# Kernel tuning notes

Hardware: AMD Instinct MI355X
Metric: run time of the kernel (lower is better)

The kernel has to match this reference:

```python
import jax, jax.numpy as jnp
import numpy as np

N_NODES = 100000
N_EDGES = 1600000
D_FEAT = 64


def setup_inputs() -> dict:
    key = jax.random.key(0)
    k1, k2, k3 = jax.random.split(key, 3)
    h = jax.random.normal(k1, (N_NODES, D_FEAT), dtype=jnp.float32)
    src = jax.random.randint(k2, (N_EDGES,), 0, N_NODES, dtype=jnp.int32)
    dst = jax.random.randint(k3, (N_EDGES,), 0, N_NODES, dtype=jnp.int32)
    edge_index = jnp.stack([src, dst], axis=0)  # [2, E]
    return {"h": h, "edge_index": edge_index}


def reference(h, edge_index):
    # EdgePassing: message = src node features (gather along edges)
    # Max_aggregation: per-dst-node max over incoming messages (segment max)
    src, dst = edge_index[0], edge_index[1]
    msgs = h[src]  # [E, D] gathered mailbox, never densified per-node
    agg = jax.ops.segment_max(msgs, dst, num_segments=N_NODES)  # [N, D]
    # DGL leaves nodes with no incoming messages at zero; segment_max yields -inf
    return jnp.where(jnp.isneginf(agg), jnp.zeros_like(agg), agg)
```

## Files before the change

kernel.cpp:

```cpp
#include <hip/hip_runtime.h>
#include <stdint.h>

#define D_FEAT 64
#define NEG_INF_BITS 0xFF800000u
#define ENC_NEG_INF  0x007FFFFFu
#define NPB 64
#define BSHIFT 6
#define BM_BLOCK 256
#define MAXB 2048
#define PL_BLOCKS 64
#define PL_THREADS 1024

__device__ __forceinline__ unsigned enc_f32(float v) {
    unsigned b = __float_as_uint(v);
    return ((int)b >= 0) ? (b ^ 0x80000000u) : ~b;
}
__device__ __forceinline__ unsigned dec_bits(unsigned u) {
    if (u == ENC_NEG_INF) return 0u;
    return (u & 0x80000000u) ? (u ^ 0x80000000u) : ~u;
}

__global__ void hist_kernel(const int* __restrict__ dst, int* __restrict__ hist,
                            int E, int B, int aligned4) {
    __shared__ int lh[MAXB];
    for (int i = threadIdx.x; i < B; i += blockDim.x) lh[i] = 0;
    __syncthreads();
    int gid = blockIdx.x * blockDim.x + threadIdx.x;
    int gstride = gridDim.x * blockDim.x;
    int n4 = aligned4 ? (E >> 2) : 0;
    const int4* d4 = (const int4*)dst;
    for (int k = gid; k < n4; k += gstride) {
        int4 d = d4[k];
        atomicAdd(&lh[d.x >> BSHIFT], 1);
        atomicAdd(&lh[d.y >> BSHIFT], 1);
        atomicAdd(&lh[d.z >> BSHIFT], 1);
        atomicAdd(&lh[d.w >> BSHIFT], 1);
    }
    for (int i = (n4 << 2) + gid; i < E; i += gstride)
        atomicAdd(&lh[dst[i] >> BSHIFT], 1);
    __syncthreads();
    for (int i = threadIdx.x; i < B; i += blockDim.x) {
        int c = lh[i];
        if (c) atomicAdd(&hist[i], c);
    }
}

__global__ void scan_kernel(const int* __restrict__ hist, int* __restrict__ bucket_start,
                            int* __restrict__ cursor, int B) {
    __shared__ int lds[MAXB / 2];
    int tid = threadIdx.x;
    int i0 = 2 * tid, i1 = 2 * tid + 1;
    int v0 = (i0 < B) ? hist[i0] : 0;
    int v1 = (i1 < B) ? hist[i1] : 0;
    int s = v0 + v1;
    lds[tid] = s;
    __syncthreads();
    for (int off = 1; off < (MAXB / 2); off <<= 1) {
        int t = (tid >= off) ? lds[tid - off] : 0;
        __syncthreads();
        lds[tid] += t;
        __syncthreads();
    }
    int excl = lds[tid] - s;
    if (i0 < B) { bucket_start[i0] = excl;      cursor[i0] = excl; }
    if (i1 < B) { bucket_start[i1] = excl + v0; cursor[i1] = excl + v0; }
    if (tid == (MAXB / 2) - 1) bucket_start[B] = lds[tid];
}

__global__ void __launch_bounds__(PL_THREADS)
place_kernel(const int* __restrict__ src, const int* __restrict__ dst,
             int* __restrict__ cursor, unsigned* __restrict__ packed,
             int E, int Te, int B, int aligned4) {
    __shared__ int lh[MAXB];
    int t = blockIdx.x;
    int beg = t * Te;
    int end = min(E, beg + Te);
    if (beg >= end) return;
    for (int i = threadIdx.x; i < B; i += blockDim.x) lh[i] = 0;
    __syncthreads();
    int nE = end - beg;
    int n4 = aligned4 ? (nE >> 2) : 0;
    const int4* d4 = (const int4*)(dst + beg);
    const int4* s4 = (const int4*)(src + beg);
    for (int k = threadIdx.x; k < n4; k += blockDim.x) {
        int4 d = d4[k];
        atomicAdd(&lh[d.x >> BSHIFT], 1);
        atomicAdd(&lh[d.y >> BSHIFT], 1);
        atomicAdd(&lh[d.z >> BSHIFT], 1);
        atomicAdd(&lh[d.w >> BSHIFT], 1);
    }
    for (int i = beg + (n4 << 2) + threadIdx.x; i < end; i += blockDim.x)
        atomicAdd(&lh[dst[i] >> BSHIFT], 1);
    __syncthreads();
    for (int i = threadIdx.x; i < B; i += blockDim.x) {
        int c = lh[i];
        lh[i] = c ? atomicAdd(&cursor[i], c) : 0;
    }
    __syncthreads();
    for (int k = threadIdx.x; k < n4; k += blockDim.x) {
        int4 d = d4[k];
        int4 s = s4[k];
        int p0 = atomicAdd(&lh[d.x >> BSHIFT], 1);
        packed[p0] = (unsigned)s.x | ((unsigned)(d.x & (NPB - 1)) << 17);
        int p1 = atomicAdd(&lh[d.y >> BSHIFT], 1);
        packed[p1] = (unsigned)s.y | ((unsigned)(d.y & (NPB - 1)) << 17);
        int p2 = atomicAdd(&lh[d.z >> BSHIFT], 1);
        packed[p2] = (unsigned)s.z | ((unsigned)(d.z & (NPB - 1)) << 17);
        int p3 = atomicAdd(&lh[d.w >> BSHIFT], 1);
        packed[p3] = (unsigned)s.w | ((unsigned)(d.w & (NPB - 1)) << 17);
    }
    for (int i = beg + (n4 << 2) + threadIdx.x; i < end; i += blockDim.x) {
        int d = dst[i];
        int pos = atomicAdd(&lh[d >> BSHIFT], 1);
        packed[pos] = (unsigned)src[i] | ((unsigned)(d & (NPB - 1)) << 17);
    }
}

__global__ void __launch_bounds__(BM_BLOCK)
bucket_max_kernel(const float* __restrict__ h,
                  const int* __restrict__ bucket_start,
                  const unsigned* __restrict__ packed,
                  float* __restrict__ out, int N) {
    __shared__ unsigned buf[NPB * D_FEAT];
    int b = blockIdx.x;
    int tid = threadIdx.x;
    int node0 = b << BSHIFT;
    int nvals = (min(NPB, N - node0)) * D_FEAT;

    for (int i = tid; i < NPB * D_FEAT; i += BM_BLOCK) buf[i] = ENC_NEG_INF;
    __syncthreads();

    int beg = bucket_start[b];
    int end = bucket_start[b + 1];
    int wid = tid >> 6;
    int lane = tid & 63;

    for (int base = beg + (wid << 6); base < end; base += BM_BLOCK) {
        int nk = min(64, end - base);
        unsigned p = (lane < nk) ? packed[base + lane] : 0u;
        int j = 0;
        for (; j + 8 <= nk; j += 8) {
            unsigned q[8];
            float v[8];
            #pragma unroll
            for (int k = 0; k < 8; ++k) q[k] = (unsigned)__shfl((int)p, j + k);
            #pragma unroll
            for (int k = 0; k < 8; ++k) v[k] = h[(size_t)(q[k] & 0x1FFFFu) * D_FEAT + lane];
            #pragma unroll
            for (int k = 0; k < 8; ++k)
                atomicMax(&buf[(q[k] >> 17) * D_FEAT + lane], enc_f32(v[k]));
        }
        for (; j < nk; ++j) {
            unsigned pj = (unsigned)__shfl((int)p, j);
            float v = h[(size_t)(pj & 0x1FFFFu) * D_FEAT + lane];
            atomicMax(&buf[(pj >> 17) * D_FEAT + lane], enc_f32(v));
        }
    }
    __syncthreads();

    if (nvals == NPB * D_FEAT) {
        uint4* o4 = (uint4*)(out + (size_t)node0 * D_FEAT);
        const uint4* b4 = (const uint4*)buf;
        for (int i = tid; i < (NPB * D_FEAT) / 4; i += BM_BLOCK) {
            uint4 u = b4[i];
            uint4 r;
            r.x = dec_bits(u.x); r.y = dec_bits(u.y);
            r.z = dec_bits(u.z); r.w = dec_bits(u.w);
            o4[i] = r;
        }
    } else {
        unsigned* o = (unsigned*)(out + (size_t)node0 * D_FEAT);
        for (int i = tid; i < nvals; i += BM_BLOCK) o[i] = dec_bits(buf[i]);
    }
}

__global__ void init_out_kernel(uint4* __restrict__ out, int n4) {
    int i = blockIdx.x * blockDim.x + threadIdx.x;
    if (i < n4) {
        uint4 v;
        v.x = NEG_INF_BITS; v.y = NEG_INF_BITS; v.z = NEG_INF_BITS; v.w = NEG_INF_BITS;
        out[i] = v;
    }
}
__global__ void scatter_max_kernel(const float* __restrict__ h, const int* __restrict__ src,
                                   const int* __restrict__ dst, float* __restrict__ out, int E) {
    int gid = blockIdx.x * blockDim.x + threadIdx.x;
    int e = gid >> 6;
    if (e >= E) return;
    int lane = gid & 63;
    float v = h[src[e] * D_FEAT + lane];
    int* addr = (int*)(out + dst[e] * D_FEAT + lane);
    if (v >= 0.0f) atomicMax(addr, __float_as_int(v));
    else           atomicMin((unsigned int*)addr, __float_as_uint(v));
}
__global__ void finalize_kernel(float* __restrict__ out, int n) {
    int i = blockIdx.x * blockDim.x + threadIdx.x;
    if (i < n && __float_as_uint(out[i]) == NEG_INF_BITS) out[i] = 0.0f;
}

extern "C" void kernel_launch(void* const* d_in, const int* in_sizes, int n_in,
                              void* d_out, int out_size, void* d_ws, size_t ws_size,
                              hipStream_t stream) {
    const float* h = (const float*)d_in[0];
    const int* edge_index = (const int*)d_in[1];
    int E = in_sizes[1] / 2;
    const int* src = edge_index;
    const int* dst = edge_index + E;
    float* out = (float*)d_out;
    int N = out_size / D_FEAT;

    int B = (N + NPB - 1) >> BSHIFT;
    size_t need = ((size_t)3 * B + 1 + (size_t)E) * sizeof(int);

    if (N <= (1 << 17) && B <= MAXB && E > 0 && ws_size >= need) {
        int* hist         = (int*)d_ws;
        int* bucket_start = hist + B;
        int* cursor       = bucket_start + B + 1;
        unsigned* packed  = (unsigned*)(cursor + B);

        int aligned4 = (((((uintptr_t)dst) | ((uintptr_t)src)) & 15) == 0) ? 1 : 0;

        hipMemsetAsync(hist, 0, (size_t)B * sizeof(int), stream);
        hist_kernel<<<512, 512, 0, stream>>>(dst, hist, E, B, aligned4);
        scan_kernel<<<1, MAXB / 2, 0, stream>>>(hist, bucket_start, cursor, B);
        int Te = ((E + PL_BLOCKS - 1) / PL_BLOCKS + 3) & ~3;
        place_kernel<<<PL_BLOCKS, PL_THREADS, 0, stream>>>(src, dst, cursor, packed, E, Te, B, aligned4);
        bucket_max_kernel<<<B, BM_BLOCK, 0, stream>>>(h, bucket_start, packed, out, N);
    } else {
        int n4 = out_size / 4;
        init_out_kernel<<<(n4 + 255) / 256, 256, 0, stream>>>((uint4*)out, n4);
        long long total = (long long)E * 64;
        scatter_max_kernel<<<(int)((total + 255) / 256), 256, 0, stream>>>(h, src, dst, out, E);
        finalize_kernel<<<(out_size + 255) / 256, 256, 0, stream>>>(out, out_size);
    }
}
```

Baseline: 182.2 us.

## Fuse histogram and scan via last-block reduction; deepen gather unroll

```diff
diff --git a/kernel.cpp b/kernel.cpp
--- a/kernel.cpp
+++ b/kernel.cpp
@@ -8,6 +8,8 @@
 #define BSHIFT 6
 #define BM_BLOCK 256
 #define MAXB 2048
+#define T_CNT 256
+#define CNT_THREADS 512
 #define PL_BLOCKS 64
 #define PL_THREADS 1024
 
@@ -20,51 +22,71 @@
     return (u & 0x80000000u) ? (u ^ 0x80000000u) : ~u;
 }
 
-__global__ void hist_kernel(const int* __restrict__ dst, int* __restrict__ hist,
-                            int E, int B, int aligned4) {
+__global__ void __launch_bounds__(CNT_THREADS)
+count_scan_kernel(const int* __restrict__ dst, int* __restrict__ partial,
+                  int* __restrict__ bucket_start, int* __restrict__ cursor,
+                  int* __restrict__ done,
+                  int E, int Te, int B, int Bp, int aligned4)
+{
     __shared__ int lh[MAXB];
-    for (int i = threadIdx.x; i < B; i += blockDim.x) lh[i] = 0;
-    __syncthreads();
-    int gid = blockIdx.x * blockDim.x + threadIdx.x;
-    int gstride = gridDim.x * blockDim.x;
-    int n4 = aligned4 ? (E >> 2) : 0;
-    const int4* d4 = (const int4*)dst;
-    for (int k = gid; k < n4; k += gstride) {
+    __shared__ int sums[CNT_THREADS];
+    __shared__ int swin;
+    const int tid = threadIdx.x;
+    const int t = blockIdx.x;
+
+    for (int i = tid; i < B; i += CNT_THREADS) lh[i] = 0;
+    __syncthreads();
+
+    int beg = t * Te;
+    int end = min(E, beg + Te);
+    int nE = (end > beg) ? (end - beg) : 0;
+    int n4 = aligned4 ? (nE >> 2) : 0;
+    const int4* d4 = (const int4*)(dst + beg);
+    for (int k = tid; k < n4; k += CNT_THREADS) {
         int4 d = d4[k];
         atomicAdd(&lh[d.x >> BSHIFT], 1);
         atomicAdd(&lh[d.y >> BSHIFT], 1);
         atomicAdd(&lh[d.z >> BSHIFT], 1);
         atomicAdd(&lh[d.w >> BSHIFT], 1);
     }
-    for (int i = (n4 << 2) + gid; i < E; i += gstride)
+    for (int i = beg + (n4 << 2) + tid; i < end; i += CNT_THREADS)
         atomicAdd(&lh[dst[i] >> BSHIFT], 1);
     __syncthreads();
-    for (int i = threadIdx.x; i < B; i += blockDim.x) {
-        int c = lh[i];
-        if (c) atomicAdd(&hist[i], c);
-    }
-}
-
-__global__ void scan_kernel(const int* __restrict__ hist, int* __restrict__ bucket_start,
-                            int* __restrict__ cursor, int B) {
-    __shared__ int lds[MAXB / 2];
-    int tid = threadIdx.x;
-    int i0 = 2 * tid, i1 = 2 * tid + 1;
-    int v0 = (i0 < B) ? hist[i0] : 0;
-    int v1 = (i1 < B) ? hist[i1] : 0;
-    int s = v0 + v1;
-    lds[tid] = s;
-    __syncthreads();
-    for (int off = 1; off < (MAXB / 2); off <<= 1) {
-        int t = (tid >= off) ? lds[tid - off] : 0;
+
+    for (int i = tid; i < Bp; i += CNT_THREADS)
+        partial[t * Bp + i] = (i < B) ? lh[i] : 0;
+
+    __threadfence();
+    if (tid == 0) swin = (atomicAdd(done, 1) == (int)gridDim.x - 1);
+    __syncthreads();
+    if (!swin) return;
+    __threadfence();
+
+    const int ncol4 = Bp >> 2;
+    const int4* p4 = (const int4*)partial;
+    int c0 = 0, c1 = 0, c2 = 0, c3 = 0;
+    if (tid < ncol4) {
+        for (int r = 0; r < (int)gridDim.x; ++r) {
+            int4 v = p4[(size_t)r * ncol4 + tid];
+            c0 += v.x; c1 += v.y; c2 += v.z; c3 += v.w;
+        }
+    }
+    int loc = c0 + c1 + c2 + c3;
+    sums[tid] = loc;
+    __syncthreads();
+    for (int off = 1; off < CNT_THREADS; off <<= 1) {
+        int u = (tid >= off) ? sums[tid - off] : 0;
         __syncthreads();
-        lds[tid] += t;
+        sums[tid] += u;
         __syncthreads();
     }
-    int excl = lds[tid] - s;
-    if (i0 < B) { bucket_start[i0] = excl;      cursor[i0] = excl; }
-    if (i1 < B) { bucket_start[i1] = excl + v0; cursor[i1] = excl + v0; }
-    if (tid == (MAXB / 2) - 1) bucket_start[B] = lds[tid];
+    int excl = sums[tid] - loc;
+    int i0 = tid << 2;
+    if (i0 + 0 < B) { bucket_start[i0 + 0] = excl; cursor[i0 + 0] = excl; } excl += c0;
+    if (i0 + 1 < B) { bucket_start[i0 + 1] = excl; cursor[i0 + 1] = excl; } excl += c1;
+    if (i0 + 2 < B) { bucket_start[i0 + 2] = excl; cursor[i0 + 2] = excl; } excl += c2;
+    if (i0 + 3 < B) { bucket_start[i0 + 3] = excl; cursor[i0 + 3] = excl; } excl += c3;
+    if (tid == CNT_THREADS - 1) bucket_start[B] = sums[CNT_THREADS - 1];
 }
 
 __global__ void __launch_bounds__(PL_THREADS)
@@ -116,7 +138,7 @@
     }
 }
 
-__global__ void __launch_bounds__(BM_BLOCK)
+__global__ void __launch_bounds__(BM_BLOCK, 8)
 bucket_max_kernel(const float* __restrict__ h,
                   const int* __restrict__ bucket_start,
                   const unsigned* __restrict__ packed,
@@ -139,6 +161,17 @@
         int nk = min(64, end - base);
         unsigned p = (lane < nk) ? packed[base + lane] : 0u;
         int j = 0;
+        for (; j + 16 <= nk; j += 16) {
+            unsigned q[16];
+            float v[16];
+            #pragma unroll
+            for (int k = 0; k < 16; ++k) q[k] = (unsigned)__shfl((int)p, j + k);
+            #pragma unroll
+            for (int k = 0; k < 16; ++k) v[k] = h[(size_t)(q[k] & 0x1FFFFu) * D_FEAT + lane];
+            #pragma unroll
+            for (int k = 0; k < 16; ++k)
+                atomicMax(&buf[(q[k] >> 17) * D_FEAT + lane], enc_f32(v[k]));
+        }
         for (; j + 8 <= nk; j += 8) {
             unsigned q[8];
             float v[8];
@@ -210,21 +243,28 @@
     int N = out_size / D_FEAT;
 
     int B = (N + NPB - 1) >> BSHIFT;
-    size_t need = ((size_t)3 * B + 1 + (size_t)E) * sizeof(int);
+    int Bp = (B + 3) & ~3;
+    size_t need = ((size_t)T_CNT * Bp + (B + 1) + B + 1 + (size_t)E) * sizeof(int);
 
     if (N <= (1 << 17) && B <= MAXB && E > 0 && ws_size >= need) {
-        int* hist         = (int*)d_ws;
-        int* bucket_start = hist + B;
+        int* partial      = (int*)d_ws;
+        int* bucket_start = partial + (size_t)T_CNT * Bp;
         int* cursor       = bucket_start + B + 1;
-        unsigned* packed  = (unsigned*)(cursor + B);
+        int* done         = cursor + B;
+        unsigned* packed  = (unsigned*)(done + 1);
 
         int aligned4 = (((((uintptr_t)dst) | ((uintptr_t)src)) & 15) == 0) ? 1 : 0;
 
-        hipMemsetAsync(hist, 0, (size_t)B * sizeof(int), stream);
-        hist_kernel<<<512, 512, 0, stream>>>(dst, hist, E, B, aligned4);
-        scan_kernel<<<1, MAXB / 2, 0, stream>>>(hist, bucket_start, cursor, B);
-        int Te = ((E + PL_BLOCKS - 1) / PL_BLOCKS + 3) & ~3;
-        place_kernel<<<PL_BLOCKS, PL_THREADS, 0, stream>>>(src, dst, cursor, packed, E, Te, B, aligned4);
+        hipMemsetAsync(done, 0, sizeof(int), stream);
+
+        int Te1 = ((E + T_CNT - 1) / T_CNT + 3) & ~3;
+        count_scan_kernel<<<T_CNT, CNT_THREADS, 0, stream>>>(
+            dst, partial, bucket_start, cursor, done, E, Te1, B, Bp, aligned4);
+
+        int Te2 = ((E + PL_BLOCKS - 1) / PL_BLOCKS + 3) & ~3;
+        place_kernel<<<PL_BLOCKS, PL_THREADS, 0, stream>>>(
+            src, dst, cursor, packed, E, Te2, B, aligned4);
+
         bucket_max_kernel<<<B, BM_BLOCK, 0, stream>>>(h, bucket_start, packed, out, N);
     } else {
         int n4 = out_size / 4;
```

After: 276.2 us. 51.6% more time.

## Replace histogram+scan bucketing with fixed-capacity buckets and overflow list

Applied to the files above, without the earlier changes.

```diff
diff --git a/kernel.cpp b/kernel.cpp
--- a/kernel.cpp
+++ b/kernel.cpp
@@ -8,8 +8,9 @@
 #define BSHIFT 6
 #define BM_BLOCK 256
 #define MAXB 2048
-#define PL_BLOCKS 64
-#define PL_THREADS 1024
+#define PL_BLOCKS 128
+#define PL_THREADS 512
+#define O_CAP 65536
 
 __device__ __forceinline__ unsigned enc_f32(float v) {
     unsigned b = __float_as_uint(v);
@@ -20,57 +21,12 @@
     return (u & 0x80000000u) ? (u ^ 0x80000000u) : ~u;
 }
 
-__global__ void hist_kernel(const int* __restrict__ dst, int* __restrict__ hist,
-                            int E, int B, int aligned4) {
-    __shared__ int lh[MAXB];
-    for (int i = threadIdx.x; i < B; i += blockDim.x) lh[i] = 0;
-    __syncthreads();
-    int gid = blockIdx.x * blockDim.x + threadIdx.x;
-    int gstride = gridDim.x * blockDim.x;
-    int n4 = aligned4 ? (E >> 2) : 0;
-    const int4* d4 = (const int4*)dst;
-    for (int k = gid; k < n4; k += gstride) {
-        int4 d = d4[k];
-        atomicAdd(&lh[d.x >> BSHIFT], 1);
-        atomicAdd(&lh[d.y >> BSHIFT], 1);
-        atomicAdd(&lh[d.z >> BSHIFT], 1);
-        atomicAdd(&lh[d.w >> BSHIFT], 1);
-    }
-    for (int i = (n4 << 2) + gid; i < E; i += gstride)
-        atomicAdd(&lh[dst[i] >> BSHIFT], 1);
-    __syncthreads();
-    for (int i = threadIdx.x; i < B; i += blockDim.x) {
-        int c = lh[i];
-        if (c) atomicAdd(&hist[i], c);
-    }
-}
-
-__global__ void scan_kernel(const int* __restrict__ hist, int* __restrict__ bucket_start,
-                            int* __restrict__ cursor, int B) {
-    __shared__ int lds[MAXB / 2];
-    int tid = threadIdx.x;
-    int i0 = 2 * tid, i1 = 2 * tid + 1;
-    int v0 = (i0 < B) ? hist[i0] : 0;
-    int v1 = (i1 < B) ? hist[i1] : 0;
-    int s = v0 + v1;
-    lds[tid] = s;
-    __syncthreads();
-    for (int off = 1; off < (MAXB / 2); off <<= 1) {
-        int t = (tid >= off) ? lds[tid - off] : 0;
-        __syncthreads();
-        lds[tid] += t;
-        __syncthreads();
-    }
-    int excl = lds[tid] - s;
-    if (i0 < B) { bucket_start[i0] = excl;      cursor[i0] = excl; }
-    if (i1 < B) { bucket_start[i1] = excl + v0; cursor[i1] = excl + v0; }
-    if (tid == (MAXB / 2) - 1) bucket_start[B] = lds[tid];
-}
-
 __global__ void __launch_bounds__(PL_THREADS)
 place_kernel(const int* __restrict__ src, const int* __restrict__ dst,
-             int* __restrict__ cursor, unsigned* __restrict__ packed,
-             int E, int Te, int B, int aligned4) {
+             int* __restrict__ cnt, int* __restrict__ ovf_cnt,
+             int* __restrict__ ovf_dst, int* __restrict__ ovf_src,
+             unsigned* __restrict__ packed,
+             int E, int Te, int B, int cap, int aligned4) {
     __shared__ int lh[MAXB];
     int t = blockIdx.x;
     int beg = t * Te;
@@ -94,33 +50,30 @@
     __syncthreads();
     for (int i = threadIdx.x; i < B; i += blockDim.x) {
         int c = lh[i];
-        lh[i] = c ? atomicAdd(&cursor[i], c) : 0;
-    }
-    __syncthreads();
-    for (int k = threadIdx.x; k < n4; k += blockDim.x) {
-        int4 d = d4[k];
-        int4 s = s4[k];
-        int p0 = atomicAdd(&lh[d.x >> BSHIFT], 1);
-        packed[p0] = (unsigned)s.x | ((unsigned)(d.x & (NPB - 1)) << 17);
-        int p1 = atomicAdd(&lh[d.y >> BSHIFT], 1);
-        packed[p1] = (unsigned)s.y | ((unsigned)(d.y & (NPB - 1)) << 17);
-        int p2 = atomicAdd(&lh[d.z >> BSHIFT], 1);
-        packed[p2] = (unsigned)s.z | ((unsigned)(d.z & (NPB - 1)) << 17);
-        int p3 = atomicAdd(&lh[d.w >> BSHIFT], 1);
-        packed[p3] = (unsigned)s.w | ((unsigned)(d.w & (NPB - 1)) << 17);
-    }
-    for (int i = beg + (n4 << 2) + threadIdx.x; i < end; i += blockDim.x) {
+        lh[i] = c ? atomicAdd(&cnt[i], c) : 0;
+    }
+    __syncthreads();
+    for (int i = beg + threadIdx.x; i < end; i += blockDim.x) {
         int d = dst[i];
-        int pos = atomicAdd(&lh[d >> BSHIFT], 1);
-        packed[pos] = (unsigned)src[i] | ((unsigned)(d & (NPB - 1)) << 17);
+        int s = src[i];
+        int b = d >> BSHIFT;
+        int pos = atomicAdd(&lh[b], 1);
+        if (pos < cap) {
+            packed[(size_t)b * cap + pos] = (unsigned)s | ((unsigned)(d & (NPB - 1)) << 17);
+        } else {
+            int o = atomicAdd(ovf_cnt, 1);
+            if (o < O_CAP) { ovf_dst[o] = d; ovf_src[o] = s; }
+        }
     }
 }
 
 __global__ void __launch_bounds__(BM_BLOCK)
 bucket_max_kernel(const float* __restrict__ h,
-                  const int* __restrict__ bucket_start,
+                  const int* __restrict__ cnt, const int* __restrict__ ovf_cnt,
+                  const int* __restrict__ ovf_dst, const int* __restrict__ ovf_src,
+                  const int* __restrict__ src, const int* __restrict__ dst,
                   const unsigned* __restrict__ packed,
-                  float* __restrict__ out, int N) {
+                  float* __restrict__ out, int N, int E, int cap) {
     __shared__ unsigned buf[NPB * D_FEAT];
     int b = blockIdx.x;
     int tid = threadIdx.x;
@@ -130,8 +83,9 @@
     for (int i = tid; i < NPB * D_FEAT; i += BM_BLOCK) buf[i] = ENC_NEG_INF;
     __syncthreads();
 
-    int beg = bucket_start[b];
-    int end = bucket_start[b + 1];
+    int total = cnt[b];
+    int beg = b * cap;
+    int end = beg + min(total, cap);
     int wid = tid >> 6;
     int lane = tid & 63;
 
@@ -156,6 +110,29 @@
             atomicMax(&buf[(pj >> 17) * D_FEAT + lane], enc_f32(v));
         }
     }
+
+    int ov = *ovf_cnt;
+    if (ov > 0) {
+        if (ov <= O_CAP) {
+            for (int i = 0; i < ov; ++i) {
+                int d = ovf_dst[i];
+                if ((d >> BSHIFT) == b) {
+                    float v = h[(size_t)ovf_dst[i] * 0 + (size_t)ovf_src[i] * D_FEAT + lane];
+                    atomicMax(&buf[(d & (NPB - 1)) * D_FEAT + lane], enc_f32(v));
+                }
+            }
+        } else if (total > cap) {
+            for (int e = tid; e < E; e += BM_BLOCK) {
+                int d = dst[e];
+                if ((d >> BSHIFT) == b) {
+                    const float* hr = h + (size_t)src[e] * D_FEAT;
+                    int row = (d & (NPB - 1)) * D_FEAT;
+                    for (int f = 0; f < D_FEAT; ++f)
+                        atomicMax(&buf[row + f], enc_f32(hr[f]));
+                }
+            }
+        }
+    }
     __syncthreads();
 
     if (nvals == NPB * D_FEAT) {
@@ -210,22 +187,31 @@
     int N = out_size / D_FEAT;
 
     int B = (N + NPB - 1) >> BSHIFT;
-    size_t need = ((size_t)3 * B + 1 + (size_t)E) * sizeof(int);
-
-    if (N <= (1 << 17) && B <= MAXB && E > 0 && ws_size >= need) {
-        int* hist         = (int*)d_ws;
-        int* bucket_start = hist + B;
-        int* cursor       = bucket_start + B + 1;
-        unsigned* packed  = (unsigned*)(cursor + B);
+
+    int cap = 0;
+    if (B > 0) {
+        cap = (((E / B) * 5) / 4 + 63) & ~63;
+        if (cap < 128) cap = 128;
+    }
+    size_t need = ((size_t)B + 1 + 2 * (size_t)O_CAP + (size_t)B * cap) * sizeof(int);
+
+    if (N <= (1 << 17) && B <= MAXB && E > 0 && cap > 0 && ws_size >= need) {
+        int* cnt         = (int*)d_ws;
+        int* ovf_cnt     = cnt + B;
+        int* ovf_dst     = ovf_cnt + 1;
+        int* ovf_src     = ovf_dst + O_CAP;
+        unsigned* packed = (unsigned*)(ovf_src + O_CAP);
 
         int aligned4 = (((((uintptr_t)dst) | ((uintptr_t)src)) & 15) == 0) ? 1 : 0;
 
-        hipMemsetAsync(hist, 0, (size_t)B * sizeof(int), stream);
-        hist_kernel<<<512, 512, 0, stream>>>(dst, hist, E, B, aligned4);
-        scan_kernel<<<1, MAXB / 2, 0, stream>>>(hist, bucket_start, cursor, B);
+        hipMemsetAsync(cnt, 0, (size_t)(B + 1) * sizeof(int), stream);
+
         int Te = ((E + PL_BLOCKS - 1) / PL_BLOCKS + 3) & ~3;
-        place_kernel<<<PL_BLOCKS, PL_THREADS, 0, stream>>>(src, dst, cursor, packed, E, Te, B, aligned4);
-        bucket_max_kernel<<<B, BM_BLOCK, 0, stream>>>(h, bucket_start, packed, out, N);
+        place_kernel<<<PL_BLOCKS, PL_THREADS, 0, stream>>>(
+            src, dst, cnt, ovf_cnt, ovf_dst, ovf_src, packed, E, Te, B, cap, aligned4);
+
+        bucket_max_kernel<<<B, BM_BLOCK, 0, stream>>>(
+            h, cnt, ovf_cnt, ovf_dst, ovf_src, src, dst, packed, out, N, E, cap);
     } else {
         int n4 = out_size / 4;
         init_out_kernel<<<(n4 + 255) / 256, 256, 0, stream>>>((uint4*)out, n4);
```

Result: faster. 158.7 us (-12.9%).
